# Optimization experiments

Hardware: AMD Instinct MI355X
Metric: run time of the kernel (lower is better)

Reference implementation:

```python
import jax, jax.numpy as jnp
import numpy as np

# Fixed ragged structure (embed_seqlens = [[512,512,512,512]] * 8): 32 segments of 512 tokens.
SEG = 32      # number of segments
L = 512       # tokens per segment
R = 64        # compress_rate -> queries per segment (split_integer(512,64) = [8]*64)
POOL = 8      # tokens averaged per query
H = 32        # n_heads
HD = 128      # head_dim
D = 4096      # hidden_dim
EPS = 1e-5


def rmsnorm(x, w):
    var = jnp.mean(x * x, axis=-1, keepdims=True)
    return x * jax.lax.rsqrt(var + EPS) * w


def setup_inputs() -> dict:
    key = jax.random.key(0)
    ks = jax.random.split(key, 4)
    x = jax.random.normal(ks[0], (SEG * L, D), dtype=jnp.float32)
    attn_norm_w = jnp.ones((D,), dtype=jnp.float32)
    wq = jax.random.normal(ks[1], (D, H * HD), dtype=jnp.float32) * 0.02
    wkv = jax.random.normal(ks[2], (D, 2 * H * HD), dtype=jnp.float32) * 0.02
    wo = jax.random.normal(ks[3], (H * HD, D), dtype=jnp.float32) * 0.02
    out_norm_w = jnp.ones((D,), dtype=jnp.float32)
    return {"x": x, "attn_norm_w": attn_norm_w, "wq": wq, "wkv": wkv,
            "wo": wo, "out_norm_w": out_norm_w}


def reference(x, attn_norm_w, wq, wkv, wo, out_norm_w):
    # pool_mask @ x: mean over each consecutive POOL-token group (block-diag ones(t)/t)
    queries = x.reshape(SEG * R, POOL, D).mean(axis=1)          # [SEG*R, D]
    qn = rmsnorm(queries, attn_norm_w)                          # attention_norm on queries only
    q = (qn @ wq).reshape(SEG, R, H, HD)                        # [S, R, H, HD]
    kv = x @ wkv                                                # context = raw x
    k, v = jnp.split(kv, 2, axis=-1)
    k = k.reshape(SEG, L, H, HD)
    v = v.reshape(SEG, L, H, HD)
    scale = HD ** -0.5
    # BlockDiagonalMask(q_seqlen=[R]*SEG, kv_seqlen=[L]*SEG) == per-segment dense attention
    scores = jnp.einsum("sqhd,skhd->shqk", q, k) * scale        # [S, H, R, L]
    attn = jax.nn.softmax(scores, axis=-1)
    o = jnp.einsum("shqk,skhd->sqhd", attn, v).reshape(SEG * R, H * HD)
    out = o @ wo + queries                                      # residual
    return rmsnorm(out, out_norm_w)                             # pooling_out_norm
```

## Files before the change

kernel.cpp:

```cpp
#include <hip/hip_runtime.h>
#include <hip/hip_bf16.h>

typedef _Float16 h16;
typedef _Float16 f16x8 __attribute__((ext_vector_type(8)));
typedef _Float16 f16x4 __attribute__((ext_vector_type(4)));
typedef float f32x4 __attribute__((ext_vector_type(4)));

#define SEGS 32
#define LCTX 512
#define RQ 64
#define NH 32
#define HDIM 128
#define DMODEL 4096

__global__ __launch_bounds__(256) void cast_f16_kernel(const float* __restrict__ in,
                                                       h16* __restrict__ out) {
    long i = ((long)blockIdx.x * 256 + threadIdx.x) * 4;
    float4 f = *(const float4*)&in[i];
    f16x4 o;
    o[0] = (h16)f.x; o[1] = (h16)f.y; o[2] = (h16)f.z; o[3] = (h16)f.w;
    *(f16x4*)&out[i] = o;
}

__global__ __launch_bounds__(256) void transpose_cast_kernel(const float* __restrict__ in,
                                                             h16* __restrict__ out,
                                                             int K, int N) {
    __shared__ float tile[32][33];
    int bx = blockIdx.x;
    int by = blockIdx.y;
    int tx = threadIdx.x & 31, ty = threadIdx.x >> 5;
#pragma unroll
    for (int j = 0; j < 4; j++)
        tile[ty + j * 8][tx] = in[(long)(by * 32 + ty + j * 8) * N + bx * 32 + tx];
    __syncthreads();
#pragma unroll
    for (int j = 0; j < 4; j++)
        out[(long)(bx * 32 + ty + j * 8) * K + by * 32 + tx] = (h16)tile[tx][ty + j * 8];
}

__global__ __launch_bounds__(256) void pool_rms_kernel(const float* __restrict__ x,
                                                       const float* __restrict__ wnorm,
                                                       float* __restrict__ queries,
                                                       h16* __restrict__ qn) {
    const int qi = blockIdx.x;
    const int t = threadIdx.x;
    const long base = (long)qi * 8 * DMODEL;
    float v[16];
    float ss = 0.f;
#pragma unroll
    for (int i = 0; i < 16; i++) {
        int col = t + i * 256;
        float s = 0.f;
#pragma unroll
        for (int r = 0; r < 8; r++) s += x[base + (long)r * DMODEL + col];
        v[i] = s * 0.125f;
        ss += v[i] * v[i];
    }
#pragma unroll
    for (int d = 1; d < 64; d <<= 1) ss += __shfl_xor(ss, d, 64);
    __shared__ float red[4];
    if ((t & 63) == 0) red[t >> 6] = ss;
    __syncthreads();
    float tot = red[0] + red[1] + red[2] + red[3];
    float scale = rsqrtf(tot / (float)DMODEL + 1e-5f);
#pragma unroll
    for (int i = 0; i < 16; i++) {
        int col = t + i * 256;
        queries[(long)qi * DMODEL + col] = v[i];
        qn[(long)qi * DMODEL + col] = (h16)(v[i] * scale * wnorm[col]);
    }
}


__device__ __forceinline__ void g2l16(const h16* g, char* l) {
    __builtin_amdgcn_global_load_lds(
        (const __attribute__((address_space(1))) unsigned int*)g,
        (__attribute__((address_space(3))) unsigned int*)l, 16, 0, 0);
}

#define MFMA(d, va, vb) d = __builtin_amdgcn_mfma_f32_16x16x32_f16(va, vb, d, 0, 0, 0)

#define GPHASE(OFF0, OFF1, MI0, MI1, STAGE_STMT, TAIL)                           \
    a0 = *(const f16x8*)(smem + ao + (OFF0) + kf0);                              \
    a1 = *(const f16x8*)(smem + ao + (OFF0) + kf1);                              \
    a2 = *(const f16x8*)(smem + ao + (OFF1) + kf0);                              \
    a3 = *(const f16x8*)(smem + ao + (OFF1) + kf1);                              \
    STAGE_STMT;                                                                  \
    __builtin_amdgcn_s_barrier();                                                \
    asm volatile("s_waitcnt lgkmcnt(0)" ::: "memory");                           \
    __builtin_amdgcn_sched_barrier(0);                                           \
    __builtin_amdgcn_s_setprio(1);                                               \
    MFMA(acc[MI0][0], a0, b00); MFMA(acc[MI1][0], a2, b00);                      \
    MFMA(acc[MI0][1], a0, b10); MFMA(acc[MI1][1], a2, b10);                      \
    MFMA(acc[MI0][2], a0, b20); MFMA(acc[MI1][2], a2, b20);                      \
    MFMA(acc[MI0][3], a0, b30); MFMA(acc[MI1][3], a2, b30);                      \
    MFMA(acc[MI0][0], a1, b01); MFMA(acc[MI1][0], a3, b01);                      \
    MFMA(acc[MI0][1], a1, b11); MFMA(acc[MI1][1], a3, b11);                      \
    MFMA(acc[MI0][2], a1, b21); MFMA(acc[MI1][2], a3, b21);                      \
    MFMA(acc[MI0][3], a1, b31); MFMA(acc[MI1][3], a3, b31);                      \
    __builtin_amdgcn_s_setprio(0);                                               \
    TAIL;                                                                        \
    __builtin_amdgcn_s_barrier();                                                \
    __builtin_amdgcn_sched_barrier(0)

#define LOADB(bb)                                                                \
    b00 = *(const f16x8*)(smem + (bb) + 0    + kf0);                             \
    b01 = *(const f16x8*)(smem + (bb) + 0    + kf1);                             \
    b10 = *(const f16x8*)(smem + (bb) + 2048 + kf0);                             \
    b11 = *(const f16x8*)(smem + (bb) + 2048 + kf1);                             \
    b20 = *(const f16x8*)(smem + (bb) + 4096 + kf0);                             \
    b21 = *(const f16x8*)(smem + (bb) + 4096 + kf1);                             \
    b30 = *(const f16x8*)(smem + (bb) + 6144 + kf0);                             \
    b31 = *(const f16x8*)(smem + (bb) + 6144 + kf1)

#define STAGE8()                                                                 \
    do { g2l16(gp0, smem + po + lo0); gp0 += 64;                                 \
         g2l16(gp1, smem + po + lo1); gp1 += 64;                                 \
         g2l16(gp2, smem + po + lo2); gp2 += 64;                                 \
         g2l16(gp3, smem + po + lo3); gp3 += 64;                                 \
         g2l16(gp4, smem + po + lo4); gp4 += 64;                                 \
         g2l16(gp5, smem + po + lo5); gp5 += 64;                                 \
         g2l16(gp6, smem + po + lo6); gp6 += 64;                                 \
         g2l16(gp7, smem + po + lo7); gp7 += 64; } while (0)

__global__ __launch_bounds__(512, 2) void gemm256_kernel(
    const h16* __restrict__ A, const h16* __restrict__ Bt,
    h16* __restrict__ Ch, float* __restrict__ Cf, const float* __restrict__ res,
    int M, int N, int K, int EPI) {
    __shared__ __align__(16) char smem[131072];

    const int t = threadIdx.x;
    const int lane = t & 63, w = t >> 6;
    const int wm = w >> 2, wn = w & 3;
    const int row16 = lane & 15, kq = lane >> 4;

    const int nwg = gridDim.x;
    const int id = blockIdx.x;
    const int swz = (id & 7) * (nwg >> 3) + (id >> 3);
    const int NBX = N >> 8;
    const int by = swz / NBX, bx = swz % NBX;
    const long byM = (long)by * 256, bxN = (long)bx * 256;

    const unsigned X = ((row16 & 4) ? 32u : 0u) | ((row16 & 8) ? 64u : 0u);
    const unsigned kf0 = (kq * 16) ^ X;
    const unsigned kf1 = (64 + kq * 16) ^ X;
    const unsigned aBase = wm * 16384 + row16 * 128;
    const unsigned bBase = 32768u + (wn >> 1) * 16384 + (wn & 1) * 8192 + row16 * 128;

    const unsigned t16x = (unsigned)(t * 16) ^ ((t & 32) ? 32u : 0u) ^ ((t & 64) ? 64u : 0u);
    const int rl = (int)(t16x >> 7);
    const int chh = (int)((t16x & 127) >> 1);
    const h16* gp0 = Bt + (bxN +   0 + rl) * K + chh;
    const h16* gp1 = Bt + (bxN +  64 + rl) * K + chh;
    const h16* gp2 = Bt + (bxN + 128 + rl) * K + chh;
    const h16* gp3 = Bt + (bxN + 192 + rl) * K + chh;
    const h16* gp4 = A  + (byM +   0 + rl) * K + chh;
    const h16* gp5 = A  + (byM + 128 + rl) * K + chh;
    const h16* gp6 = A  + (byM +  64 + rl) * K + chh;
    const h16* gp7 = A  + (byM + 192 + rl) * K + chh;
    const unsigned wb = (unsigned)w * 1024;
    const unsigned lo0 = 32768u + wb,         lo1 = 32768u + 8192 + wb;
    const unsigned lo2 = 49152u + wb,         lo3 = 49152u + 8192 + wb;
    const unsigned lo4 = wb,                  lo5 = 16384u + wb;
    const unsigned lo6 = 8192u + wb,          lo7 = 24576u + wb;

    g2l16(gp0, smem + lo0); gp0 += 64;
    g2l16(gp1, smem + lo1); gp1 += 64;
    g2l16(gp2, smem + lo2); gp2 += 64;
    g2l16(gp3, smem + lo3); gp3 += 64;
    g2l16(gp4, smem + lo4); gp4 += 64;
    g2l16(gp5, smem + lo5); gp5 += 64;
    g2l16(gp6, smem + lo6); gp6 += 64;
    g2l16(gp7, smem + lo7); gp7 += 64;
    asm volatile("s_waitcnt vmcnt(2)" ::: "memory");
    __builtin_amdgcn_s_barrier();
    __builtin_amdgcn_sched_barrier(0);

    f32x4 acc[8][4] = {};
    const int NT = K >> 6;
    for (int tt = 0; tt < NT - 1; ++tt) {
        const unsigned bo = (tt & 1) ? 65536u : 0u;
        const unsigned po = 65536u - bo;
        const unsigned ao = bo + aBase;
        f16x8 a0, a1, a2, a3;
        f16x8 b00, b01, b10, b11, b20, b21, b30, b31;
        LOADB(bo + bBase);
        GPHASE(0,     2048,  0, 1, STAGE8(), (void)0);
        GPHASE(4096,  6144,  2, 3, (void)0,
               asm volatile("s_waitcnt vmcnt(8)" ::: "memory"));
        GPHASE(8192,  10240, 4, 5, (void)0, (void)0);
        GPHASE(12288, 14336, 6, 7, (void)0,
               asm volatile("s_waitcnt vmcnt(2)" ::: "memory"));
    }
    {
        const unsigned bo = ((NT - 1) & 1) ? 65536u : 0u;
        const unsigned ao = bo + aBase;
        f16x8 a0, a1, a2, a3;
        f16x8 b00, b01, b10, b11, b20, b21, b30, b31;
        LOADB(bo + bBase);
        GPHASE(0,     2048,  0, 1, (void)0, (void)0);
        GPHASE(4096,  6144,  2, 3, (void)0,
               asm volatile("s_waitcnt vmcnt(0)" ::: "memory"));
        GPHASE(8192,  10240, 4, 5, (void)0, (void)0);
        GPHASE(12288, 14336, 6, 7, (void)0, (void)0);
    }

    const long wrow = byM + wm * 128 + (lane >> 4) * 4;
    const long wcol = bxN + wn * 64 + row16;
#pragma unroll
    for (int mi = 0; mi < 8; mi++)
#pragma unroll
        for (int n = 0; n < 4; n++)
#pragma unroll
            for (int r = 0; r < 4; r++) {
                long idx = (wrow + mi * 16 + r) * N + wcol + n * 16;
                float v = acc[mi][n][r];
                if (EPI == 0) Ch[idx] = (h16)v;
                else          Cf[idx] = v + res[idx];
            }
}

__global__ __launch_bounds__(256) void attn_kernel(const h16* __restrict__ q,
                                                   const h16* __restrict__ kv,
                                                   h16* __restrict__ o) {
    const int h = blockIdx.x;
    const int s = blockIdx.y;
    const int t = threadIdx.x;
    const int lane = t & 63, w = t >> 6;
    const int row16 = lane & 15, quad = lane >> 4;

    __shared__ h16 kls[32][HDIM + 8];
    __shared__ h16 vls[HDIM][32 + 8];
    __shared__ h16 pls[4][16][32 + 8];

    f16x8 qf[4];
    {
        const long qrow = (long)(s * RQ + w * 16 + row16) * DMODEL + h * HDIM;
#pragma unroll
        for (int f = 0; f < 4; f++) qf[f] = *(const f16x8*)&q[qrow + f * 32 + quad * 8];
    }
    const float sc = 0.08838834764831845f;
    f32x4 oacc[8] = {};
    float m_i[4], l_i[4];
#pragma unroll
    for (int r = 0; r < 4; r++) { m_i[r] = -1e30f; l_i[r] = 0.f; }

    const long kvbase = (long)s * LCTX * 8192 + h * HDIM;

    for (int kc = 0; kc < LCTX; kc += 32) {
#pragma unroll
        for (int p = 0; p < 2; p++) {
            int u = t + p * 256;
            int r = u >> 4;
            int c8 = (u & 15) * 8;
            *(uint4*)&kls[r][c8] = *(const uint4*)&kv[kvbase + (long)(kc + r) * 8192 + c8];
            f16x8 vv = *(const f16x8*)&kv[kvbase + 4096 + (long)(kc + r) * 8192 + c8];
#pragma unroll
            for (int j = 0; j < 8; j++) vls[c8 + j][r] = vv[j];
        }
        __syncthreads();

        f32x4 st[2] = {};
#pragma unroll
        for (int ct = 0; ct < 2; ct++)
#pragma unroll
            for (int f = 0; f < 4; f++) {
                f16x8 bk = *(const f16x8*)&kls[ct * 16 + row16][f * 32 + quad * 8];
                st[ct] = __builtin_amdgcn_mfma_f32_16x16x32_f16(qf[f], bk, st[ct], 0, 0, 0);
            }

#pragma unroll
        for (int r = 0; r < 4; r++) {
            float s0 = st[0][r] * sc, s1 = st[1][r] * sc;
            float mx = fmaxf(s0, s1);
#pragma unroll
            for (int d = 1; d < 16; d <<= 1) mx = fmaxf(mx, __shfl_xor(mx, d, 64));
            float mn = fmaxf(m_i[r], mx);
            float al = __expf(m_i[r] - mn);
            float p0 = __expf(s0 - mn), p1 = __expf(s1 - mn);
            float ps = p0 + p1;
#pragma unroll
            for (int d = 1; d < 16; d <<= 1) ps += __shfl_xor(ps, d, 64);
            l_i[r] = l_i[r] * al + ps;
            m_i[r] = mn;
#pragma unroll
            for (int ht = 0; ht < 8; ht++) oacc[ht][r] *= al;
            pls[w][quad * 4 + r][row16]      = (h16)p0;
            pls[w][quad * 4 + r][16 + row16] = (h16)p1;
        }
        f16x8 pa = *(const f16x8*)&pls[w][row16][quad * 8];
#pragma unroll
        for (int ht = 0; ht < 8; ht++) {
            f16x8 bv = *(const f16x8*)&vls[ht * 16 + row16][quad * 8];
            oacc[ht] = __builtin_amdgcn_mfma_f32_16x16x32_f16(pa, bv, oacc[ht], 0, 0, 0);
        }
        __syncthreads();
    }
#pragma unroll
    for (int r = 0; r < 4; r++) {
        float inv = 1.0f / l_i[r];
        long orow = (long)(s * RQ + w * 16 + quad * 4 + r) * DMODEL + h * HDIM;
#pragma unroll
        for (int ht = 0; ht < 8; ht++) o[orow + ht * 16 + row16] = (h16)(oacc[ht][r] * inv);
    }
}

__global__ __launch_bounds__(256) void final_rms_kernel(const float* __restrict__ tmp,
                                                        const float* __restrict__ w,
                                                        float* __restrict__ out) {
    const int row = blockIdx.x;
    const int t = threadIdx.x;
    float v[16];
    float ss = 0.f;
#pragma unroll
    for (int i = 0; i < 16; i++) {
        v[i] = tmp[(long)row * DMODEL + t + i * 256];
        ss += v[i] * v[i];
    }
#pragma unroll
    for (int d = 1; d < 64; d <<= 1) ss += __shfl_xor(ss, d, 64);
    __shared__ float red[4];
    if ((t & 63) == 0) red[t >> 6] = ss;
    __syncthreads();
    float tot = red[0] + red[1] + red[2] + red[3];
    float scale = rsqrtf(tot / (float)DMODEL + 1e-5f);
#pragma unroll
    for (int i = 0; i < 16; i++) {
        int col = t + i * 256;
        out[(long)row * DMODEL + col] = v[i] * scale * w[col];
    }
}

extern "C" void kernel_launch(void* const* d_in, const int* in_sizes, int n_in,
                              void* d_out, int out_size, void* d_ws, size_t ws_size,
                              hipStream_t stream) {
    const float* x      = (const float*)d_in[0];
    const float* anw    = (const float*)d_in[1];
    const float* wq     = (const float*)d_in[2];
    const float* wkv    = (const float*)d_in[3];
    const float* wo     = (const float*)d_in[4];
    const float* onw    = (const float*)d_in[5];
    float* out          = (float*)d_out;

    size_t off = 0;
    auto carve = [&](size_t bytes) {
        void* p = (char*)d_ws + off;
        off += (bytes + 255) & ~(size_t)255;
        return p;
    };
    h16*   xh      = (h16*)  carve((size_t)16384 * 4096 * 2);
    h16*   wqT     = (h16*)  carve((size_t)4096 * 4096 * 2);
    h16*   wkvT    = (h16*)  carve((size_t)8192 * 4096 * 2);
    h16*   woT     = (h16*)  carve((size_t)4096 * 4096 * 2);
    float* queries = (float*)carve((size_t)2048 * 4096 * 4);
    h16*   qn      = (h16*)  carve((size_t)2048 * 4096 * 2);
    h16*   qh      = (h16*)  carve((size_t)2048 * 4096 * 2);
    h16*   kvh     = (h16*)  carve((size_t)16384 * 8192 * 2);
    h16*   oh      = (h16*)  carve((size_t)2048 * 4096 * 2);
    float* tmp     = (float*)xh;

    cast_f16_kernel<<<(16384L * 4096 / 4) / 256, 256, 0, stream>>>(x, xh);
    transpose_cast_kernel<<<dim3(4096 / 32, 4096 / 32), 256, 0, stream>>>(wq, wqT, 4096, 4096);
    transpose_cast_kernel<<<dim3(8192 / 32, 4096 / 32), 256, 0, stream>>>(wkv, wkvT, 4096, 8192);
    transpose_cast_kernel<<<dim3(4096 / 32, 4096 / 32), 256, 0, stream>>>(wo, woT, 4096, 4096);

    pool_rms_kernel<<<2048, 256, 0, stream>>>(x, anw, queries, qn);

    gemm256_kernel<<<8 * 16, 512, 0, stream>>>(
        qn, wqT, qh, nullptr, nullptr, 2048, 4096, 4096, 0);

    gemm256_kernel<<<64 * 32, 512, 0, stream>>>(
        xh, wkvT, kvh, nullptr, nullptr, 16384, 8192, 4096, 0);

    attn_kernel<<<dim3(NH, SEGS), 256, 0, stream>>>(qh, kvh, oh);

    gemm256_kernel<<<8 * 16, 512, 0, stream>>>(
        oh, woT, nullptr, tmp, queries, 2048, 4096, 4096, 1);

    final_rms_kernel<<<2048, 256, 0, stream>>>(tmp, onw, out);
}
```

Before: 2.175 ms.

## Restructure GEMM main loop with one barrier per tile and prefetched A fragments

```diff
diff --git a/kernel.cpp b/kernel.cpp
--- a/kernel.cpp
+++ b/kernel.cpp
@@ -79,39 +79,19 @@
 }
 
 #define MFMA(d, va, vb) d = __builtin_amdgcn_mfma_f32_16x16x32_f16(va, vb, d, 0, 0, 0)
-
-#define GPHASE(OFF0, OFF1, MI0, MI1, STAGE_STMT, TAIL)                           \
-    a0 = *(const f16x8*)(smem + ao + (OFF0) + kf0);                              \
-    a1 = *(const f16x8*)(smem + ao + (OFF0) + kf1);                              \
-    a2 = *(const f16x8*)(smem + ao + (OFF1) + kf0);                              \
-    a3 = *(const f16x8*)(smem + ao + (OFF1) + kf1);                              \
-    STAGE_STMT;                                                                  \
-    __builtin_amdgcn_s_barrier();                                                \
-    asm volatile("s_waitcnt lgkmcnt(0)" ::: "memory");                           \
-    __builtin_amdgcn_sched_barrier(0);                                           \
+#define RD(off) (*(const f16x8*)(smem + (off)))
+
+#define CLUSTER(MI0, MI1, x0, x1, x2, x3)                                        \
     __builtin_amdgcn_s_setprio(1);                                               \
-    MFMA(acc[MI0][0], a0, b00); MFMA(acc[MI1][0], a2, b00);                      \
-    MFMA(acc[MI0][1], a0, b10); MFMA(acc[MI1][1], a2, b10);                      \
-    MFMA(acc[MI0][2], a0, b20); MFMA(acc[MI1][2], a2, b20);                      \
-    MFMA(acc[MI0][3], a0, b30); MFMA(acc[MI1][3], a2, b30);                      \
-    MFMA(acc[MI0][0], a1, b01); MFMA(acc[MI1][0], a3, b01);                      \
-    MFMA(acc[MI0][1], a1, b11); MFMA(acc[MI1][1], a3, b11);                      \
-    MFMA(acc[MI0][2], a1, b21); MFMA(acc[MI1][2], a3, b21);                      \
-    MFMA(acc[MI0][3], a1, b31); MFMA(acc[MI1][3], a3, b31);                      \
-    __builtin_amdgcn_s_setprio(0);                                               \
-    TAIL;                                                                        \
-    __builtin_amdgcn_s_barrier();                                                \
-    __builtin_amdgcn_sched_barrier(0)
-
-#define LOADB(bb)                                                                \
-    b00 = *(const f16x8*)(smem + (bb) + 0    + kf0);                             \
-    b01 = *(const f16x8*)(smem + (bb) + 0    + kf1);                             \
-    b10 = *(const f16x8*)(smem + (bb) + 2048 + kf0);                             \
-    b11 = *(const f16x8*)(smem + (bb) + 2048 + kf1);                             \
-    b20 = *(const f16x8*)(smem + (bb) + 4096 + kf0);                             \
-    b21 = *(const f16x8*)(smem + (bb) + 4096 + kf1);                             \
-    b30 = *(const f16x8*)(smem + (bb) + 6144 + kf0);                             \
-    b31 = *(const f16x8*)(smem + (bb) + 6144 + kf1)
+    MFMA(acc[MI0][0], x0, b00); MFMA(acc[MI1][0], x2, b00);                      \
+    MFMA(acc[MI0][1], x0, b10); MFMA(acc[MI1][1], x2, b10);                      \
+    MFMA(acc[MI0][2], x0, b20); MFMA(acc[MI1][2], x2, b20);                      \
+    MFMA(acc[MI0][3], x0, b30); MFMA(acc[MI1][3], x2, b30);                      \
+    MFMA(acc[MI0][0], x1, b01); MFMA(acc[MI1][0], x3, b01);                      \
+    MFMA(acc[MI0][1], x1, b11); MFMA(acc[MI1][1], x3, b11);                      \
+    MFMA(acc[MI0][2], x1, b21); MFMA(acc[MI1][2], x3, b21);                      \
+    MFMA(acc[MI0][3], x1, b31); MFMA(acc[MI1][3], x3, b31);                      \
+    __builtin_amdgcn_s_setprio(0)
 
 #define STAGE8()                                                                 \
     do { g2l16(gp0, smem + po + lo0); gp0 += 64;                                 \
@@ -164,45 +144,45 @@
     const unsigned lo4 = wb,                  lo5 = 16384u + wb;
     const unsigned lo6 = 8192u + wb,          lo7 = 24576u + wb;
 
-    g2l16(gp0, smem + lo0); gp0 += 64;
-    g2l16(gp1, smem + lo1); gp1 += 64;
-    g2l16(gp2, smem + lo2); gp2 += 64;
-    g2l16(gp3, smem + lo3); gp3 += 64;
-    g2l16(gp4, smem + lo4); gp4 += 64;
-    g2l16(gp5, smem + lo5); gp5 += 64;
-    g2l16(gp6, smem + lo6); gp6 += 64;
-    g2l16(gp7, smem + lo7); gp7 += 64;
-    asm volatile("s_waitcnt vmcnt(2)" ::: "memory");
-    __builtin_amdgcn_s_barrier();
-    __builtin_amdgcn_sched_barrier(0);
+    {
+        const unsigned po = 0u;
+        STAGE8();
+    }
 
     f32x4 acc[8][4] = {};
     const int NT = K >> 6;
-    for (int tt = 0; tt < NT - 1; ++tt) {
-        const unsigned bo = (tt & 1) ? 65536u : 0u;
-        const unsigned po = 65536u - bo;
-        const unsigned ao = bo + aBase;
-        f16x8 a0, a1, a2, a3;
-        f16x8 b00, b01, b10, b11, b20, b21, b30, b31;
-        LOADB(bo + bBase);
-        GPHASE(0,     2048,  0, 1, STAGE8(), (void)0);
-        GPHASE(4096,  6144,  2, 3, (void)0,
-               asm volatile("s_waitcnt vmcnt(8)" ::: "memory"));
-        GPHASE(8192,  10240, 4, 5, (void)0, (void)0);
-        GPHASE(12288, 14336, 6, 7, (void)0,
-               asm volatile("s_waitcnt vmcnt(2)" ::: "memory"));
-    }
-    {
-        const unsigned bo = ((NT - 1) & 1) ? 65536u : 0u;
-        const unsigned ao = bo + aBase;
-        f16x8 a0, a1, a2, a3;
-        f16x8 b00, b01, b10, b11, b20, b21, b30, b31;
-        LOADB(bo + bBase);
-        GPHASE(0,     2048,  0, 1, (void)0, (void)0);
-        GPHASE(4096,  6144,  2, 3, (void)0,
-               asm volatile("s_waitcnt vmcnt(0)" ::: "memory"));
-        GPHASE(8192,  10240, 4, 5, (void)0, (void)0);
-        GPHASE(12288, 14336, 6, 7, (void)0, (void)0);
+    for (int tt = 0; tt < NT; ++tt) {
+        const unsigned bo = (tt & 1) ? 0u : 65536u;
+        const unsigned rb = (tt & 1) ? 65536u : 0u;
+        (void)bo;
+        const unsigned po = 65536u - rb;
+        const unsigned ao = rb + aBase;
+        const unsigned bb = rb + bBase;
+
+        __syncthreads();
+        if (tt + 1 < NT) STAGE8();
+
+        f16x8 b00 = RD(bb + 0    + kf0), b01 = RD(bb + 0    + kf1);
+        f16x8 b10 = RD(bb + 2048 + kf0), b11 = RD(bb + 2048 + kf1);
+        f16x8 b20 = RD(bb + 4096 + kf0), b21 = RD(bb + 4096 + kf1);
+        f16x8 b30 = RD(bb + 6144 + kf0), b31 = RD(bb + 6144 + kf1);
+        f16x8 p0a0 = RD(ao + 0     + kf0), p0a1 = RD(ao + 0     + kf1);
+        f16x8 p0a2 = RD(ao + 2048  + kf0), p0a3 = RD(ao + 2048  + kf1);
+        f16x8 p1a0 = RD(ao + 4096  + kf0), p1a1 = RD(ao + 4096  + kf1);
+        f16x8 p1a2 = RD(ao + 6144  + kf0), p1a3 = RD(ao + 6144  + kf1);
+
+        CLUSTER(0, 1, p0a0, p0a1, p0a2, p0a3);
+
+        f16x8 p2a0 = RD(ao + 8192  + kf0), p2a1 = RD(ao + 8192  + kf1);
+        f16x8 p2a2 = RD(ao + 10240 + kf0), p2a3 = RD(ao + 10240 + kf1);
+
+        CLUSTER(2, 3, p1a0, p1a1, p1a2, p1a3);
+
+        f16x8 p3a0 = RD(ao + 12288 + kf0), p3a1 = RD(ao + 12288 + kf1);
+        f16x8 p3a2 = RD(ao + 14336 + kf0), p3a3 = RD(ao + 14336 + kf1);
+
+        CLUSTER(4, 5, p2a0, p2a1, p2a2, p2a3);
+        CLUSTER(6, 7, p3a0, p3a1, p3a2, p3a3);
     }
 
     const long wrow = byM + wm * 128 + (lane >> 4) * 4;
```

Result: faster. 2.014 ms (-7.4%).
